# Kernel optimization log

Hardware: AMD Instinct MI355X
Metric: run time of the kernel (lower is better)

Reference implementation:

```python
import jax, jax.numpy as jnp
import numpy as np

B, T = 64, 2048
VOCAB, H, OUT = 32000, 256, 256


def setup_inputs() -> dict:
    key = jax.random.key(0)
    ks = jax.random.split(key, 6)
    x = jax.random.randint(ks[0], (B, T), 0, VOCAB, dtype=jnp.int32)
    embed = jax.random.normal(ks[1], (VOCAB, H), dtype=jnp.float32) * 0.02
    # torch Linear(h+h, h): weight [h, 2h]; we store transposed [2h, h]
    W_fc = jax.random.normal(ks[2], (2 * H, H), dtype=jnp.float32) * (1.0 / np.sqrt(2 * H))
    b_fc = jax.random.normal(ks[3], (H,), dtype=jnp.float32) * 0.01
    W_out = jax.random.normal(ks[4], (H, OUT), dtype=jnp.float32) * (1.0 / np.sqrt(H))
    b_out = jax.random.normal(ks[5], (OUT,), dtype=jnp.float32) * 0.01
    return {"x": x, "embed": embed, "W_fc": W_fc, "b_fc": b_fc, "W_out": W_out, "b_out": b_out}


def reference(x, embed, W_fc, b_fc, W_out, b_out):
    # SimpleRNN.forward_bptt: h_t = tanh(fc(concat([embed(x_t), h_{t-1}])))
    # concat-linear split: fc([e, h]) = e @ Wx + h @ Wh + b
    h_dim = embed.shape[1]
    Wx, Wh = W_fc[:h_dim], W_fc[h_dim:]
    xe = embed[x]                                   # [B, T, H] gather
    xproj = jnp.einsum('bth,hk->btk', xe, Wx) + b_fc  # precompute input projection

    def step(h, xp_t):
        h_new = jnp.tanh(xp_t + h @ Wh)
        return h_new, h_new

    h0 = jnp.zeros((x.shape[0], h_dim), dtype=embed.dtype)
    h_last, hs = jax.lax.scan(step, h0, jnp.swapaxes(xproj, 0, 1))  # hs: [T, B, H]
    hs = jnp.swapaxes(hs, 0, 1)                     # [B, T, H] = stack(hs[1:], dim=1)
    out = h_last @ W_out + b_out                    # [B, OUT]
    return out, hs
```

## Files before the change

### kernel.cpp

```cpp
#include <hip/hip_runtime.h>

#define RNN_T 2048
#define RNN_B 64
#define RNN_H 256
#define KSTR 20

typedef float v2f __attribute__((ext_vector_type(2)));

__global__ __launch_bounds__(256)
void xproj_kernel(const int* __restrict__ x, const float* __restrict__ embed,
                  const float* __restrict__ Wfc, const float* __restrict__ bfc,
                  float* __restrict__ hsb) {
    __shared__ int ixs[64];
    __shared__ __align__(16) float A[64][260];
    const int tid = threadIdx.x;
    const long rb0 = (long)blockIdx.x * 64;

    if (tid < 64) ixs[tid] = x[rb0 + tid];
    __syncthreads();

    {
        const int r = tid >> 2, q = tid & 3;
        const float* erow = embed + (long)ixs[r] * RNN_H;
        #pragma unroll
        for (int i = 0; i < 16; ++i) {
            const int c = q * 64 + i * 4;
            *(float4*)&A[r][c] = *(const float4*)(erow + c);
        }
    }
    __syncthreads();

    const int tj = tid & 31, tr = tid >> 5;
    const int r0 = tr * 8, j0 = tj * 4, j1 = 128 + tj * 4;

    float acc[8][8];
    #pragma unroll
    for (int i = 0; i < 8; ++i)
        #pragma unroll
        for (int c = 0; c < 8; ++c) acc[i][c] = 0.f;

    for (int k4 = 0; k4 < 64; ++k4) {
        float4 a[8];
        #pragma unroll
        for (int i = 0; i < 8; ++i) a[i] = *(const float4*)&A[r0 + i][k4 * 4];
        #pragma unroll
        for (int kk = 0; kk < 4; ++kk) {
            const int k = k4 * 4 + kk;
            const float4 wa = *(const float4*)(Wfc + (long)k * RNN_H + j0);
            const float4 wb = *(const float4*)(Wfc + (long)k * RNN_H + j1);
            #pragma unroll
            for (int i = 0; i < 8; ++i) {
                const float av = reinterpret_cast<const float*>(&a[i])[kk];
                acc[i][0] = fmaf(av, wa.x, acc[i][0]);
                acc[i][1] = fmaf(av, wa.y, acc[i][1]);
                acc[i][2] = fmaf(av, wa.z, acc[i][2]);
                acc[i][3] = fmaf(av, wa.w, acc[i][3]);
                acc[i][4] = fmaf(av, wb.x, acc[i][4]);
                acc[i][5] = fmaf(av, wb.y, acc[i][5]);
                acc[i][6] = fmaf(av, wb.z, acc[i][6]);
                acc[i][7] = fmaf(av, wb.w, acc[i][7]);
            }
        }
    }

    const float4 ba = *(const float4*)(bfc + j0);
    const float4 bb = *(const float4*)(bfc + j1);
    #pragma unroll
    for (int i = 0; i < 8; ++i) {
        const long row = rb0 + r0 + i;
        float4 o1 = make_float4(acc[i][0] + ba.x, acc[i][1] + ba.y,
                                acc[i][2] + ba.z, acc[i][3] + ba.w);
        float4 o2 = make_float4(acc[i][4] + bb.x, acc[i][5] + bb.y,
                                acc[i][6] + bb.z, acc[i][7] + bb.w);
        *(float4*)(hsb + row * RNN_H + j0) = o1;
        *(float4*)(hsb + row * RNN_H + j1) = o2;
    }
}

#define DPP_HOP(val, CTRL)                                                  \
    __int_as_float(__builtin_amdgcn_update_dpp(                             \
        0, __float_as_int(val), CTRL, 0xf, 0xf, true))

__device__ __forceinline__ v2f lo2(const float4 v) { return (v2f){v.x, v.y}; }
__device__ __forceinline__ v2f hi2(const float4 v) { return (v2f){v.z, v.w}; }

__global__ __launch_bounds__(512, 2)
void rnn_scan_kernel(const float* __restrict__ Wfc, const float* __restrict__ Wout,
                     const float* __restrict__ bout, float* __restrict__ out,
                     float* __restrict__ hsb) {
    __shared__ __align__(16) float hA[16 * KSTR];
    __shared__ __align__(16) float hB[16 * KSTR];
    const int tid = threadIdx.x;
    const int b = blockIdx.x;
    const int w = tid >> 6, l = tid & 63;
    const int cg = w * 4 + (l >> 4);
    const int s  = l & 15;
    const int c0 = cg * 8;
    const int k0 = s * 16;

    const float* Wh = Wfc + RNN_H * RNN_H;
    v2f wv[8][8];
    #pragma unroll
    for (int m = 0; m < 8; ++m) {
        const long kb = (long)(k0 + 2 * m) * RNN_H;
        #pragma unroll
        for (int c = 0; c < 8; ++c) {
            v2f t;
            t.x = Wh[kb + c0 + c];
            t.y = Wh[kb + RNN_H + c0 + c];
            wv[c][m] = t;
        }
    }
    #pragma unroll
    for (int m = 0; m < 8; ++m)
        asm volatile("" : "+v"(wv[0][m]), "+v"(wv[1][m]), "+v"(wv[2][m]), "+v"(wv[3][m]),
                          "+v"(wv[4][m]), "+v"(wv[5][m]), "+v"(wv[6][m]), "+v"(wv[7][m]));

    if (tid < 16 * KSTR) hA[tid] = 0.f;

    float* xpb = hsb + (long)b * RNN_T * RNN_H;
    const bool wr = ((s & 4) == 0);
    const int jcol = c0 + ((s & 3) | ((s & 8) ? 4 : 0));
    const int widx = (jcol >> 4) * KSTR + (jcol & 15);
    float* xw = xpb + jcol;
    const float* xpf = xpb + jcol + 2 * RNN_H;
    const float* xend = xpb + (long)RNN_T * RNN_H;

    float xr = 0.f, xn = 0.f;
    if (wr) { xr = xpb[jcol]; xn = xpb[RNN_H + jcol]; }
    __syncthreads();

    const float4* rdA = (const float4*)(hA + s * KSTR);
    const float4* rdB = (const float4*)(hB + s * KSTR);
    const bool m1 = (l & 1), m2 = (l & 2), m8 = (l & 8);

#define RNN_STEP(RD, WDST)                                                  \
    {                                                                       \
        float xf = 0.f;                                                     \
        if (wr && xpf < xend) xf = *xpf;                                    \
        xpf += RNN_H;                                                       \
        const float4 q0 = RD[0], q1 = RD[1], q2 = RD[2], q3 = RD[3];        \
        const v2f hp[8] = { lo2(q0), hi2(q0), lo2(q1), hi2(q1),             \
                            lo2(q2), hi2(q2), lo2(q3), hi2(q3) };           \
        v2f a0={0,0},a1={0,0},a2={0,0},a3={0,0},                            \
            a4={0,0},a5={0,0},a6={0,0},a7={0,0};                            \
        _Pragma("unroll")                                                   \
        for (int m = 0; m < 8; ++m) {                                       \
            a0 = __builtin_elementwise_fma(hp[m], wv[0][m], a0);            \
            a1 = __builtin_elementwise_fma(hp[m], wv[1][m], a1);            \
            a2 = __builtin_elementwise_fma(hp[m], wv[2][m], a2);            \
            a3 = __builtin_elementwise_fma(hp[m], wv[3][m], a3);            \
            a4 = __builtin_elementwise_fma(hp[m], wv[4][m], a4);            \
            a5 = __builtin_elementwise_fma(hp[m], wv[5][m], a5);            \
            a6 = __builtin_elementwise_fma(hp[m], wv[6][m], a6);            \
            a7 = __builtin_elementwise_fma(hp[m], wv[7][m], a7);            \
        }                                                                   \
        float s0=a0.x+a0.y, s1=a1.x+a1.y, s2=a2.x+a2.y, s3=a3.x+a3.y;       \
        float s4=a4.x+a4.y, s5=a5.x+a5.y, s6=a6.x+a6.y, s7=a7.x+a7.y;       \
                                \
        float b0 = (m1 ? s1 : s0) + DPP_HOP(m1 ? s0 : s1, 0xB1);            \
        float b1 = (m1 ? s3 : s2) + DPP_HOP(m1 ? s2 : s3, 0xB1);            \
        float b2 = (m1 ? s5 : s4) + DPP_HOP(m1 ? s4 : s5, 0xB1);            \
        float b3 = (m1 ? s7 : s6) + DPP_HOP(m1 ? s6 : s7, 0xB1);            \
                                \
        float c0v = (m2 ? b1 : b0) + DPP_HOP(m2 ? b0 : b1, 0x4E);           \
        float c1v = (m2 ? b3 : b2) + DPP_HOP(m2 ? b2 : b3, 0x4E);           \
                     \
        float dv = (m8 ? c1v : c0v) + DPP_HOP(m8 ? c0v : c1v, 0x128);       \
                    \
        dv += DPP_HOP(DPP_HOP(dv, 0x1B), 0x141);                            \
        if (wr) {                                                           \
            const float vsum = dv + xr;                                     \
            const float e = __expf(2.f * vsum);                             \
            const float hn = 1.f - 2.f * __builtin_amdgcn_rcpf(e + 1.f);    \
            WDST[widx] = hn;                                                \
            *xw = hn;                                                       \
            xr = xn; xn = xf;                                               \
        }                                                                   \
        xw += RNN_H;                                                        \
        __syncthreads();                                                    \
    }

    for (int t = 0; t < RNN_T; t += 2) {
        RNN_STEP(rdA, hB);
        RNN_STEP(rdB, hA);
    }
#undef RNN_STEP

    if (tid < RNN_H) {
        float a0 = 0.f, a1 = 0.f, a2 = 0.f, a3 = 0.f;
        for (int k = 0; k < RNN_H; k += 4) {
            const int kb = (k >> 4) * KSTR + (k & 15);
            a0 = fmaf(hA[kb + 0], Wout[(long)(k + 0) * RNN_H + tid], a0);
            a1 = fmaf(hA[kb + 1], Wout[(long)(k + 1) * RNN_H + tid], a1);
            a2 = fmaf(hA[kb + 2], Wout[(long)(k + 2) * RNN_H + tid], a2);
            a3 = fmaf(hA[kb + 3], Wout[(long)(k + 3) * RNN_H + tid], a3);
        }
        out[(long)b * RNN_H + tid] = a0 + a1 + a2 + a3 + bout[tid];
    }
}

extern "C" void kernel_launch(void* const* d_in, const int* in_sizes, int n_in,
                              void* d_out, int out_size, void* d_ws, size_t ws_size,
                              hipStream_t stream) {
    const int*   x     = (const int*)d_in[0];
    const float* embed = (const float*)d_in[1];
    const float* Wfc   = (const float*)d_in[2];
    const float* bfc   = (const float*)d_in[3];
    const float* Wout  = (const float*)d_in[4];
    const float* bout  = (const float*)d_in[5];

    float* out = (float*)d_out;
    float* hsb = out + RNN_B * RNN_H;

    xproj_kernel<<<(RNN_B * RNN_T) / 64, 256, 0, stream>>>(x, embed, Wfc, bfc, hsb);
    rnn_scan_kernel<<<RNN_B, 512, 0, stream>>>(Wfc, Wout, bout, out, hsb);
}
```

Measured before the change: 1.329 ms.

## Split RNN scan across 1024 threads with 4 columns per lane group

Doubles the scan block to 1024 threads so each 16-lane group owns 4 output columns instead of 8. This halves per-thread Wh registers and FMAs per step and drops one DPP reduction level, which shortens the per-step critical path. It also replaces __syncthreads with a custom lgkmcnt wait plus s_barrier and moves the register-pinning asm into the loop. The cost is a 16-wave barrier every timestep and fewer lanes doing useful writes.

```diff
diff --git a/kernel.cpp b/kernel.cpp
--- a/kernel.cpp
+++ b/kernel.cpp
@@ -84,7 +84,9 @@
 __device__ __forceinline__ v2f lo2(const float4 v) { return (v2f){v.x, v.y}; }
 __device__ __forceinline__ v2f hi2(const float4 v) { return (v2f){v.z, v.w}; }
 
-__global__ __launch_bounds__(512, 2)
+#define LDS_BARRIER() asm volatile("s_waitcnt lgkmcnt(0)\n\ts_barrier" ::: "memory")
+
+__global__ __launch_bounds__(1024, 4)
 void rnn_scan_kernel(const float* __restrict__ Wfc, const float* __restrict__ Wout,
                      const float* __restrict__ bout, float* __restrict__ out,
                      float* __restrict__ hsb) {
@@ -93,34 +95,30 @@
     const int tid = threadIdx.x;
     const int b = blockIdx.x;
     const int w = tid >> 6, l = tid & 63;
+    const int s  = l & 15;
     const int cg = w * 4 + (l >> 4);
-    const int s  = l & 15;
-    const int c0 = cg * 8;
+    const int c0 = cg * 4;
     const int k0 = s * 16;
 
     const float* Wh = Wfc + RNN_H * RNN_H;
-    v2f wv[8][8];
+    v2f wv[4][8];
     #pragma unroll
     for (int m = 0; m < 8; ++m) {
         const long kb = (long)(k0 + 2 * m) * RNN_H;
         #pragma unroll
-        for (int c = 0; c < 8; ++c) {
+        for (int c = 0; c < 4; ++c) {
             v2f t;
             t.x = Wh[kb + c0 + c];
             t.y = Wh[kb + RNN_H + c0 + c];
             wv[c][m] = t;
         }
     }
-    #pragma unroll
-    for (int m = 0; m < 8; ++m)
-        asm volatile("" : "+v"(wv[0][m]), "+v"(wv[1][m]), "+v"(wv[2][m]), "+v"(wv[3][m]),
-                          "+v"(wv[4][m]), "+v"(wv[5][m]), "+v"(wv[6][m]), "+v"(wv[7][m]));
 
     if (tid < 16 * KSTR) hA[tid] = 0.f;
 
     float* xpb = hsb + (long)b * RNN_T * RNN_H;
-    const bool wr = ((s & 4) == 0);
-    const int jcol = c0 + ((s & 3) | ((s & 8) ? 4 : 0));
+    const bool wr = (s < 4);
+    const int jcol = c0 + (s & 3);
     const int widx = (jcol >> 4) * KSTR + (jcol & 15);
     float* xw = xpb + jcol;
     const float* xpf = xpb + jcol + 2 * RNN_H;
@@ -132,7 +130,7 @@
 
     const float4* rdA = (const float4*)(hA + s * KSTR);
     const float4* rdB = (const float4*)(hB + s * KSTR);
-    const bool m1 = (l & 1), m2 = (l & 2), m8 = (l & 8);
+    const bool m1 = (l & 1), m2 = (l & 2);
 
 #define RNN_STEP(RD, WDST)                                                  \
     {                                                                       \
@@ -142,35 +140,27 @@
         const float4 q0 = RD[0], q1 = RD[1], q2 = RD[2], q3 = RD[3];        \
         const v2f hp[8] = { lo2(q0), hi2(q0), lo2(q1), hi2(q1),             \
                             lo2(q2), hi2(q2), lo2(q3), hi2(q3) };           \
-        v2f a0={0,0},a1={0,0},a2={0,0},a3={0,0},                            \
-            a4={0,0},a5={0,0},a6={0,0},a7={0,0};                            \
+        v2f a0={0,0}, a1={0,0}, a2={0,0}, a3={0,0};                         \
         _Pragma("unroll")                                                   \
         for (int m = 0; m < 8; ++m) {                                       \
             a0 = __builtin_elementwise_fma(hp[m], wv[0][m], a0);            \
             a1 = __builtin_elementwise_fma(hp[m], wv[1][m], a1);            \
             a2 = __builtin_elementwise_fma(hp[m], wv[2][m], a2);            \
             a3 = __builtin_elementwise_fma(hp[m], wv[3][m], a3);            \
-            a4 = __builtin_elementwise_fma(hp[m], wv[4][m], a4);            \
-            a5 = __builtin_elementwise_fma(hp[m], wv[5][m], a5);            \
-            a6 = __builtin_elementwise_fma(hp[m], wv[6][m], a6);            \
-            a7 = __builtin_elementwise_fma(hp[m], wv[7][m], a7);            \
         }                                                                   \
-        float s0=a0.x+a0.y, s1=a1.x+a1.y, s2=a2.x+a2.y, s3=a3.x+a3.y;       \
-        float s4=a4.x+a4.y, s5=a5.x+a5.y, s6=a6.x+a6.y, s7=a7.x+a7.y;       \
+        float s0 = a0.x + a0.y, s1 = a1.x + a1.y;                           \
+        float s2 = a2.x + a2.y, s3 = a3.x + a3.y;                           \
                                 \
         float b0 = (m1 ? s1 : s0) + DPP_HOP(m1 ? s0 : s1, 0xB1);            \
         float b1 = (m1 ? s3 : s2) + DPP_HOP(m1 ? s2 : s3, 0xB1);            \
-        float b2 = (m1 ? s5 : s4) + DPP_HOP(m1 ? s4 : s5, 0xB1);            \
-        float b3 = (m1 ? s7 : s6) + DPP_HOP(m1 ? s6 : s7, 0xB1);            \
                                 \
-        float c0v = (m2 ? b1 : b0) + DPP_HOP(m2 ? b0 : b1, 0x4E);           \
-        float c1v = (m2 ? b3 : b2) + DPP_HOP(m2 ? b2 : b3, 0x4E);           \
-                     \
-        float dv = (m8 ? c1v : c0v) + DPP_HOP(m8 ? c0v : c1v, 0x128);       \
+        float cv = (m2 ? b1 : b0) + DPP_HOP(m2 ? b0 : b1, 0x4E);            \
+                                    \
+        cv += DPP_HOP(cv, 0x128);                                           \
                     \
-        dv += DPP_HOP(DPP_HOP(dv, 0x1B), 0x141);                            \
+        cv += DPP_HOP(DPP_HOP(cv, 0x1B), 0x141);                            \
         if (wr) {                                                           \
-            const float vsum = dv + xr;                                     \
+            const float vsum = cv + xr;                                     \
             const float e = __expf(2.f * vsum);                             \
             const float hn = 1.f - 2.f * __builtin_amdgcn_rcpf(e + 1.f);    \
             WDST[widx] = hn;                                                \
@@ -178,12 +168,16 @@
             xr = xn; xn = xf;                                               \
         }                                                                   \
         xw += RNN_H;                                                        \
-        __syncthreads();                                                    \
+        LDS_BARRIER();                                                      \
     }
 
     for (int t = 0; t < RNN_T; t += 2) {
         RNN_STEP(rdA, hB);
         RNN_STEP(rdB, hA);
+        #pragma unroll
+        for (int m = 0; m < 8; ++m)
+            asm volatile("" : "+v"(wv[0][m]), "+v"(wv[1][m]),
+                              "+v"(wv[2][m]), "+v"(wv[3][m]));
     }
 #undef RNN_STEP
 
@@ -214,5 +208,5 @@
     float* hsb = out + RNN_B * RNN_H;
 
     xproj_kernel<<<(RNN_B * RNN_T) / 64, 256, 0, stream>>>(x, embed, Wfc, bfc, hsb);
-    rnn_scan_kernel<<<RNN_B, 512, 0, stream>>>(Wfc, Wout, bout, out, hsb);
+    rnn_scan_kernel<<<RNN_B, 1024, 0, stream>>>(Wfc, Wout, bout, out, hsb);
 }
```

After: 1.422 ms. 7.0% more time.
